# Performance work log

Measured on AMD Instinct MI355X. Metric: run time of the kernel, lower is better.

The kernel has to match this reference:

```python
import jax, jax.numpy as jnp
import numpy as np

B, K, D, H, V = 4096, 64, 128, 2048, 10000
EPS = 1e-5


def _project_ball(x):
    # map arbitrary vectors strictly inside the unit Poincare ball
    n = jnp.linalg.norm(x, axis=-1, keepdims=True)
    return 0.9 * x / (1.0 + n)


def setup_inputs() -> dict:
    key = jax.random.key(0)
    ks = jax.random.split(key, 12)
    type_embeddings = _project_ball(jax.random.normal(ks[0], (B, D), jnp.float32))
    neighbor_indexes = jax.random.randint(ks[1], (B, K), 0, V, jnp.int32)
    one_hot_neighbor_types = jnp.round(jax.random.uniform(ks[2], (B, K), jnp.float32))
    frequencies = jax.random.randint(ks[3], (V,), 1, 100000).astype(jnp.float32)
    type_lut = _project_ball(jax.random.normal(ks[4], (V, D), jnp.float32))
    IN = D + K * (D + 4 + 1)  # 8640
    s = 0.02
    W1 = jax.random.normal(ks[5], (IN, H), jnp.float32) * s
    b1 = jnp.zeros((H,), jnp.float32)
    Wh1 = jax.random.normal(ks[6], (H, H), jnp.float32) * s
    bh1 = jnp.zeros((H,), jnp.float32)
    Wh2 = jax.random.normal(ks[7], (H, H), jnp.float32) * s
    bh2 = jnp.zeros((H,), jnp.float32)
    W2 = jax.random.normal(ks[8], (H, K), jnp.float32) * s
    b2 = jnp.zeros((K,), jnp.float32)
    return dict(type_embeddings=type_embeddings, neighbor_indexes=neighbor_indexes,
                one_hot_neighbor_types=one_hot_neighbor_types, frequencies=frequencies,
                type_lut=type_lut, W1=W1, b1=b1, Wh1=Wh1, bh1=bh1, Wh2=Wh2, bh2=bh2,
                W2=W2, b2=b2)


def _forward(type_embeddings, neighbor_indexes, one_hot_neighbor_types, frequencies,
             type_lut, W1, b1, Wh1, bh1, Wh2, bh2, W2, b2):
    # embedding gather: [B, K, D]
    v = type_lut[neighbor_indexes]
    u = type_embeddings[:, None, :]  # [B, 1, D] broadcasts against [B, K, D]

    # extra features, all [B, K]
    squ = jnp.sum(u * u, axis=-1)
    sqv = jnp.sum(v * v, axis=-1)
    diff = u - v
    sqdist = jnp.sum(diff * diff, axis=-1)
    x = 1.0 + 2.0 * sqdist / ((1.0 - squ) * (1.0 - sqv))
    x = jnp.maximum(x, 1.0 + EPS)
    poincare = jnp.log(x + jnp.sqrt(x * x - 1.0))  # arccosh(x)

    dot = jnp.sum(u * v, axis=-1)
    cos = dot / jnp.maximum(jnp.sqrt(squ) * jnp.sqrt(sqv), 1e-8)
    summ = u + v
    polarization = (jnp.sum(summ * summ, axis=-1) - sqdist) / 4.0

    popularity = jnp.log1p(frequencies[neighbor_indexes])  # vectorized gather + log1p

    extra = jnp.stack([poincare, cos, polarization, dot], axis=-1)  # [B, K, 4]
    neighbor_rep = jnp.concatenate([v, extra, popularity[..., None]], axis=-1)  # [B, K, D+5]
    neighbor_rep = neighbor_rep.reshape(type_embeddings.shape[0], -1)
    inp = jnp.concatenate([type_embeddings, neighbor_rep], axis=-1)  # [B, D+K*(D+5)]

    h = jax.nn.relu(inp @ W1 + b1)        # dropout is identity at eval
    h = jax.nn.relu(h @ Wh1 + bh1)
    h = jax.nn.relu(h @ Wh2 + bh2)
    logits = h @ W2 + b2                  # [B, K]
    distribution = jax.nn.sigmoid(logits)

    t = one_hot_neighbor_types
    # stable BCE-with-logits, mean reduction
    loss = jnp.mean(jnp.maximum(logits, 0.0) - logits * t + jnp.log1p(jnp.exp(-jnp.abs(logits))))
    return distribution, loss


def reference(type_embeddings, neighbor_indexes, one_hot_neighbor_types, frequencies,
              type_lut, W1, b1, Wh1, bh1, Wh2, bh2, W2, b2):
    return _forward(type_embeddings, neighbor_indexes, one_hot_neighbor_types, frequencies,
                    type_lut, W1, b1, Wh1, bh1, Wh2, bh2, W2, b2)
```

## Files before the change

kernel.cpp:

```cpp
#include <hip/hip_runtime.h>

typedef unsigned short u16;
typedef unsigned int   u32;
typedef __attribute__((ext_vector_type(8))) __bf16 bf16x8;
typedef __attribute__((ext_vector_type(4))) float  f32x4;
typedef __attribute__((ext_vector_type(4))) u32    u32x4;

#define AS1 __attribute__((address_space(1)))
#define AS3 __attribute__((address_space(3)))


__device__ __forceinline__ u16 f2bf(float f) {
  return __builtin_bit_cast(u16, (__bf16)f);
}
__device__ __forceinline__ u32 pk2(float x, float y) {
  return (u32)__builtin_bit_cast(u16, (__bf16)x) |
         ((u32)__builtin_bit_cast(u16, (__bf16)y) << 16);
}

__device__ __forceinline__ float wred(float v) {
#pragma unroll
  for (int off = 32; off > 0; off >>= 1) v += __shfl_xor(v, off, 64);
  return v;
}

__device__ __forceinline__ void stage16(const u16* g, u16* l) {
  __builtin_amdgcn_global_load_lds((const AS1 void*)g, (AS3 void*)l, 16, 0, 0);
}

__device__ __forceinline__ int w1_orig_row(int p) {
  if (p < 128) return p;
  if (p < 8320) { int q = p - 128;  return 128 + (q >> 7) * 133 + (q & 127); }
  if (p < 8576) { int q = p - 8320; return 128 + (q >> 2) * 133 + 128 + (q & 3); }
  return 128 + (p - 8576) * 133 + 132;
}

__device__ __forceinline__ void w1_tile(const float* __restrict__ in,
                                        u16* __restrict__ out, int tile,
                                        u16 (*ls)[68], int t)
{
  const int p0 = (tile >> 5) << 6;
  const int h0 = (tile & 31) << 6;
  const int hl = t & 63, q = t >> 6;
  float v[16];
#pragma unroll
  for (int i = 0; i < 16; i++) {
    int pl = q * 16 + i;
    int orig = w1_orig_row(p0 + pl);
    v[i] = in[(size_t)orig * 2048 + h0 + hl];
  }
#pragma unroll
  for (int i = 0; i < 4; i++) {
    uint2 pk;
    pk.x = pk2(v[i * 4 + 0], v[i * 4 + 1]);
    pk.y = pk2(v[i * 4 + 2], v[i * 4 + 3]);
    *(uint2*)&ls[hl][q * 16 + i * 4] = pk;
  }
  __syncthreads();
  const int pp = t & 15, hq = t >> 4;
#pragma unroll
  for (int i = 0; i < 4; i++) {
    int hc = i * 16 + hq;
    uint2 vv = *(const uint2*)&ls[hc][pp * 4];
    *(uint2*)&out[(size_t)(h0 + hc) * 8640 + p0 + pp * 4] = vv;
  }
}

__device__ __forceinline__ void conv_tile(const float* __restrict__ in,
                                          u16* __restrict__ out, int R, int C,
                                          int tile, u16 (*ls)[68], int t)
{
  const int tiles_c = C >> 6;
  const int r0 = (tile / tiles_c) << 6;
  const int c0 = (tile % tiles_c) << 6;
  const int cl = t & 63, q = t >> 6;
  float v[16];
#pragma unroll
  for (int i = 0; i < 16; i++) {
    int rl = q * 16 + i;
    v[i] = in[(size_t)(r0 + rl) * C + c0 + cl];
  }
#pragma unroll
  for (int i = 0; i < 4; i++) {
    uint2 pk;
    pk.x = pk2(v[i * 4 + 0], v[i * 4 + 1]);
    pk.y = pk2(v[i * 4 + 2], v[i * 4 + 3]);
    *(uint2*)&ls[cl][q * 16 + i * 4] = pk;
  }
  __syncthreads();
  const int pp = t & 15, cq = t >> 4;
#pragma unroll
  for (int i = 0; i < 4; i++) {
    int cc = i * 16 + cq;
    uint2 vv = *(const uint2*)&ls[cc][pp * 4];
    *(uint2*)&out[(size_t)(c0 + cc) * R + r0 + pp * 4] = vv;
  }
}

__global__ __launch_bounds__(256) void prep_kernel(
    const float* __restrict__ W1,  u16* __restrict__ w1t,
    const float* __restrict__ Wh1, u16* __restrict__ wh1t,
    const float* __restrict__ Wh2, u16* __restrict__ wh2t,
    const float* __restrict__ W2,  u16* __restrict__ w2t,
    const float* __restrict__ te, const int* __restrict__ nidx,
    const float* __restrict__ freq, const float* __restrict__ lut,
    u16* __restrict__ inp)
{
  __shared__ u16 ls[64][68];
  __shared__ float u_sh[128];
  __shared__ float squ_sh;
  const int bid = blockIdx.x, t = threadIdx.x;
  if (bid < 4320)      { w1_tile(W1, w1t, bid, ls, t); return; }
  if (bid < 5344)      { conv_tile(Wh1, wh1t, 2048, 2048, bid - 4320, ls, t); return; }
  if (bid < 6368)      { conv_tile(Wh2, wh2t, 2048, 2048, bid - 5344, ls, t); return; }
  if (bid < 6400)      { conv_tile(W2,  w2t,  2048, 64,   bid - 6368, ls, t); return; }

  const int b = bid - 6400;
  const int l = t & 63, w = t >> 6;
  if (t < 128) u_sh[t] = te[(size_t)b * 128 + t];
  __syncthreads();
  if (w == 0) {
    float p = u_sh[l] * u_sh[l] + u_sh[l + 64] * u_sh[l + 64];
    p = wred(p);
    if (l == 0) squ_sh = p;
  }
  const size_t rb = (size_t)b * 8640;
  if (t < 64) {
    float2 u2 = *(const float2*)&u_sh[t * 2];
    *(u32*)&inp[rb + t * 2] = pk2(u2.x, u2.y);
  }
  __syncthreads();

  const float squ = squ_sh;
  const float rsq = 1.0f - squ;
  const float2 u2 = *(const float2*)&u_sh[l * 2];

#pragma unroll
  for (int mk = 0; mk < 4; ++mk) {
    const int kbase = w * 16 + mk * 4;
    int idx[4]; float2 v2[4]; float sqv[4], dot[4];
#pragma unroll
    for (int j = 0; j < 4; j++) {
      idx[j] = nidx[b * 64 + kbase + j];
      v2[j] = *(const float2*)&lut[(size_t)idx[j] * 128 + l * 2];
    }
#pragma unroll
    for (int j = 0; j < 4; j++) {
      sqv[j] = v2[j].x * v2[j].x + v2[j].y * v2[j].y;
      dot[j] = u2.x * v2[j].x + u2.y * v2[j].y;
    }
#pragma unroll
    for (int off = 32; off > 0; off >>= 1) {
#pragma unroll
      for (int j = 0; j < 4; j++) {
        sqv[j] += __shfl_xor(sqv[j], off, 64);
        dot[j] += __shfl_xor(dot[j], off, 64);
      }
    }
#pragma unroll
    for (int j = 0; j < 4; j++)
      *(u32*)&inp[rb + 128 + (size_t)(kbase + j) * 128 + l * 2] = pk2(v2[j].x, v2[j].y);

    const int js = l & 3;
    const float sv = (js & 2) ? ((js & 1) ? sqv[3] : sqv[2]) : ((js & 1) ? sqv[1] : sqv[0]);
    const float dt = (js & 2) ? ((js & 1) ? dot[3] : dot[2]) : ((js & 1) ? dot[1] : dot[0]);
    const int   ix = (js & 2) ? ((js & 1) ? idx[3] : idx[2]) : ((js & 1) ? idx[1] : idx[0]);
    const float sqd = squ + sv - 2.0f * dt;
    float x = 1.0f + 2.0f * sqd / (rsq * (1.0f - sv));
    x = fmaxf(x, 1.0f + 1e-5f);
    const float poin = logf(x + sqrtf(x * x - 1.0f));
    const float cosv = dt / fmaxf(sqrtf(squ * sv), 1e-8f);
    if (l < 4) {
      *(u32*)&inp[rb + 8320 + (kbase + l) * 4]     = pk2(poin, cosv);
      *(u32*)&inp[rb + 8320 + (kbase + l) * 4 + 2] = pk2(dt, dt);
      inp[rb + 8576 + kbase + l] = f2bf(log1pf(freq[ix]));
    }
  }
}

__global__ __launch_bounds__(256, 2) void gemm2b(
    const u16* __restrict__ A, const u16* __restrict__ BT,
    const float* __restrict__ bias, u16* __restrict__ out,
    int N, int Kd)
{
  extern __shared__ u16 lds[];
  const int t = threadIdx.x, l = t & 63, w = t >> 6;
  const int nb = N >> 7;
  const int cpx = gridDim.x >> 3;
  const int bid = (blockIdx.x & 7) * cpx + (blockIdx.x >> 3);
  const int bm = bid / nb, bn = bid % nb;
  const int m0 = bm << 7, n0 = bn << 7;
  const int vm = w >> 1, vn = w & 1;

  const size_t lda = (size_t)Kd;
  const int NT = Kd >> 6;

  const int sr = l >> 3;
  const int q  = (l & 7) ^ sr;
  const u16* sA = A  + (size_t)(m0 + w * 32 + sr) * lda + q * 8;
  const u16* sB = BT + (size_t)(n0 + w * 32 + sr) * lda + q * 8;
  const int dW = w * 2048;

  const int rl = l & 15;
  const int c0 = ((0 + (l >> 4)) ^ (rl & 7)) * 8;
  const int c1 = ((4 + (l >> 4)) ^ (rl & 7)) * 8;
  const int aBase = (vm * 64 + rl) * 64;
  const int bBase = 8192 + (vn * 64 + rl) * 64;

  f32x4 acc[4][4] = {};
  bf16x8 a0[4], a1[4], b0[4], b1[4];

  auto stageT = [&](int o, int tt) {
    const size_t kt = (size_t)tt * 64;
#pragma unroll
    for (int i = 0; i < 4; i++) {
      stage16(sA + (size_t)i * 8 * lda + kt, lds + o + dW + i * 512);
      stage16(sB + (size_t)i * 8 * lda + kt, lds + o + 8192 + dW + i * 512);
    }
  };
  auto mmq = [&](const bf16x8* a, const bf16x8* b) {
    __builtin_amdgcn_s_setprio(1);
#pragma unroll
    for (int mi = 0; mi < 4; mi++)
#pragma unroll
      for (int ni = 0; ni < 4; ni++)
        acc[mi][ni] = __builtin_amdgcn_mfma_f32_16x16x32_bf16(a[mi], b[ni], acc[mi][ni], 0, 0, 0);
    __builtin_amdgcn_s_setprio(0);
  };

  stageT(0, 0);

  for (int ti = 0; ti < NT; ++ti) {
    const int o  = (ti & 1) ? 16384 : 0;
    const int on = o ^ 16384;
    asm volatile("s_waitcnt vmcnt(0)" ::: "memory");
    __builtin_amdgcn_s_barrier();
#pragma unroll
    for (int x = 0; x < 4; x++) b0[x] = *(const bf16x8*)&lds[o + bBase + x * 1024 + c0];
#pragma unroll
    for (int x = 0; x < 4; x++) a0[x] = *(const bf16x8*)&lds[o + aBase + x * 1024 + c0];
#pragma unroll
    for (int x = 0; x < 4; x++) b1[x] = *(const bf16x8*)&lds[o + bBase + x * 1024 + c1];
#pragma unroll
    for (int x = 0; x < 4; x++) a1[x] = *(const bf16x8*)&lds[o + aBase + x * 1024 + c1];
    if (ti + 1 < NT) stageT(on, ti + 1);
    asm volatile("s_waitcnt lgkmcnt(8)" ::: "memory");
    __builtin_amdgcn_sched_barrier(0);
    mmq(a0, b0);
    asm volatile("s_waitcnt lgkmcnt(0)" ::: "memory");
    __builtin_amdgcn_sched_barrier(0);
    mmq(a1, b1);
  }

  const int rq = l >> 4, rl2 = l & 15;
#pragma unroll
  for (int mi = 0; mi < 4; mi++) {
#pragma unroll
    for (int ni = 0; ni < 4; ni++) {
      const int col = n0 + vn * 64 + ni * 16 + rl2;
      const float bv = bias[col];
#pragma unroll
      for (int j = 0; j < 4; j++) {
        const int row = m0 + vm * 64 + mi * 16 + rq * 4 + j;
        float vv = acc[mi][ni][j] + bv;
        out[(size_t)row * N + col] = f2bf(fmaxf(vv, 0.0f));
      }
    }
  }
}

__global__ __launch_bounds__(256, 2) void gemm4_part(
    const u16* __restrict__ A, const u16* __restrict__ BT,
    float* __restrict__ pbuf)
{
  __shared__ u16 lsA[2 * 128 * 32];
  __shared__ u16 lsB[2 * 64 * 32];
  const int t = threadIdx.x, l = t & 63, w = t >> 6;
  const int bmx = blockIdx.x & 31, sk = blockIdx.x >> 5;
  const int m0 = bmx << 7, k0 = sk << 9;
  float* pout = pbuf + (size_t)sk * 262144;
  const int wm = w >> 1, wn = w & 1;

  f32x4 acc[4][2] = {};
  const int srow = l >> 2, scol = (l & 3) * 8;

  const u16* pA0 = A  + (size_t)(m0 + w * 16 + srow)      * 2048 + scol + k0;
  const u16* pA1 = A  + (size_t)(m0 + 64 + w * 16 + srow) * 2048 + scol + k0;
  const u16* pB0 = BT + (size_t)(w * 16 + srow)           * 2048 + scol + k0;

  auto stage = [&](int buf, int kt) {
    u16* dA = lsA + buf * 4096;
    u16* dB = lsB + buf * 2048;
    stage16(pA0 + kt, dA + w * 512);
    stage16(pA1 + kt, dA + 2048 + w * 512);
    stage16(pB0 + kt, dB + w * 512);
  };

  stage(0, 0);
  __syncthreads();

  const int kk = (l >> 4) * 8;
  const int rl = l & 15;
  int cur = 0;
  for (int kt = 0; kt < 512; kt += 32) {
    if (kt + 32 < 512) stage(cur ^ 1, kt + 32);
    const u16* sA = lsA + cur * 4096;
    const u16* sB = lsB + cur * 2048;
    bf16x8 a[4], bb[2];
#pragma unroll
    for (int mi = 0; mi < 4; mi++)
      a[mi] = *(const bf16x8*)&sA[(wm * 64 + mi * 16 + rl) * 32 + kk];
#pragma unroll
    for (int ni = 0; ni < 2; ni++)
      bb[ni] = *(const bf16x8*)&sB[(wn * 32 + ni * 16 + rl) * 32 + kk];
#pragma unroll
    for (int mi = 0; mi < 4; mi++)
#pragma unroll
      for (int ni = 0; ni < 2; ni++)
        acc[mi][ni] = __builtin_amdgcn_mfma_f32_16x16x32_bf16(a[mi], bb[ni], acc[mi][ni], 0, 0, 0);
    __syncthreads();
    cur ^= 1;
  }

  const int rq = l >> 4, rl2 = l & 15;
#pragma unroll
  for (int mi = 0; mi < 4; mi++)
#pragma unroll
    for (int ni = 0; ni < 2; ni++) {
      const int col = wn * 32 + ni * 16 + rl2;
#pragma unroll
      for (int j = 0; j < 4; j++) {
        const int row = m0 + wm * 64 + mi * 16 + rq * 4 + j;
        pout[(size_t)row * 64 + col] = acc[mi][ni][j];
      }
    }
}

__global__ __launch_bounds__(256) void gemm4_combine(
    const float* __restrict__ pbuf, const float* __restrict__ bias,
    const float* __restrict__ oneh, float* __restrict__ dist,
    float* __restrict__ part2)
{
  __shared__ float red[256];
  const int t = threadIdx.x;
  const size_t base = (size_t)blockIdx.x * 1024 + t * 4;
  f32x4 s = *(const f32x4*)&pbuf[base];
  s += *(const f32x4*)&pbuf[base + 262144];
  s += *(const f32x4*)&pbuf[base + 524288];
  s += *(const f32x4*)&pbuf[base + 786432];
  const int col0 = (int)(base & 63);
  f32x4 th = *(const f32x4*)&oneh[base];
  float lsum = 0.0f;
  f32x4 dv;
#pragma unroll
  for (int j = 0; j < 4; j++) {
    const float x = s[j] + bias[col0 + j];
    dv[j] = 1.0f / (1.0f + expf(-x));
    lsum += fmaxf(x, 0.0f) - x * th[j] + log1pf(expf(-fabsf(x)));
  }
  *(f32x4*)&dist[base] = dv;
  red[t] = lsum;
  __syncthreads();
  for (int s2 = 128; s2 > 0; s2 >>= 1) {
    if (t < s2) red[t] += red[t + s2];
    __syncthreads();
  }
  if (t == 0) part2[blockIdx.x] = red[0];
}

__global__ void loss_final(const float* __restrict__ part2, float* __restrict__ outloss) {
  const int l = threadIdx.x;
  float v = 0.0f;
#pragma unroll
  for (int i = 0; i < 4; i++) v += part2[l + i * 64];
  v = wred(v);
  if (l == 0) outloss[0] = v * (1.0f / 262144.0f);
}

extern "C" void kernel_launch(void* const* d_in, const int* in_sizes, int n_in,
                              void* d_out, int out_size, void* d_ws, size_t ws_size,
                              hipStream_t stream)
{
  const float* te   = (const float*)d_in[0];
  const int*   nidx = (const int*)  d_in[1];
  const float* oneh = (const float*)d_in[2];
  const float* freq = (const float*)d_in[3];
  const float* lut  = (const float*)d_in[4];
  const float* W1   = (const float*)d_in[5];
  const float* b1   = (const float*)d_in[6];
  const float* Wh1  = (const float*)d_in[7];
  const float* bh1  = (const float*)d_in[8];
  const float* Wh2  = (const float*)d_in[9];
  const float* bh2  = (const float*)d_in[10];
  const float* W2   = (const float*)d_in[11];
  const float* b2   = (const float*)d_in[12];

  float* dist  = (float*)d_out;
  float* lossp = dist + 262144;

  size_t off = 0;
  char* base = (char*)d_ws;
  auto alloc = [&](size_t bytes) { char* p = base + off; off += (bytes + 255) & ~(size_t)255; return p; };
  u16* inp   = (u16*)alloc((size_t)4096 * 8640 * 2);
  u16* w1t   = (u16*)alloc((size_t)2048 * 8640 * 2);
  u16* wh1t  = (u16*)alloc((size_t)2048 * 2048 * 2);
  u16* wh2t  = (u16*)alloc((size_t)2048 * 2048 * 2);
  u16* w2t   = (u16*)alloc((size_t)64 * 2048 * 2);
  u16* h1    = (u16*)alloc((size_t)4096 * 2048 * 2);
  float* part2 = (float*)alloc(1024);
  u16* h2 = inp;
  u16* h3 = w1t;
  float* pbuf = (float*)wh1t;
  if (off > ws_size) return;

  (void)hipFuncSetAttribute((const void*)gemm2b,
                            hipFuncAttributeMaxDynamicSharedMemorySize, 65536);

  prep_kernel<<<10496, 256, 0, stream>>>(W1, w1t, Wh1, wh1t, Wh2, wh2t, W2, w2t,
                                         te, nidx, freq, lut, inp);

  gemm2b<<<512, 256, 65536, stream>>>(inp, w1t, b1, h1, 2048, 8640);
  gemm2b<<<512, 256, 65536, stream>>>(h1, wh1t, bh1, h2, 2048, 2048);
  gemm2b<<<512, 256, 65536, stream>>>(h2, wh2t, bh2, h3, 2048, 2048);
  gemm4_part   <<<128, 256, 0, stream>>>(h3, w2t, pbuf);
  gemm4_combine<<<256, 256, 0, stream>>>(pbuf, b2, oneh, dist, part2);
  loss_final   <<<1, 64, 0, stream>>>(part2, lossp);
}
```

Measured before the change: 268.1 us.

## Split K across wave pairs in GEMM tile with LDS reduction

```diff
diff --git a/kernel.cpp b/kernel.cpp
--- a/kernel.cpp
+++ b/kernel.cpp
@@ -178,7 +178,7 @@
   }
 }
 
-__global__ __launch_bounds__(256, 2) void gemm2b(
+__global__ __launch_bounds__(256, 2) void gemm2k(
     const u16* __restrict__ A, const u16* __restrict__ BT,
     const float* __restrict__ bias, u16* __restrict__ out,
     int N, int Kd)
@@ -190,7 +190,7 @@
   const int bid = (blockIdx.x & 7) * cpx + (blockIdx.x >> 3);
   const int bm = bid / nb, bn = bid % nb;
   const int m0 = bm << 7, n0 = bn << 7;
-  const int vm = w >> 1, vn = w & 1;
+  const int kg = w >> 1, vn = w & 1;
 
   const size_t lda = (size_t)Kd;
   const int NT = Kd >> 6;
@@ -202,13 +202,12 @@
   const int dW = w * 2048;
 
   const int rl = l & 15;
-  const int c0 = ((0 + (l >> 4)) ^ (rl & 7)) * 8;
-  const int c1 = ((4 + (l >> 4)) ^ (rl & 7)) * 8;
-  const int aBase = (vm * 64 + rl) * 64;
+  const int cK = ((kg * 4 + (l >> 4)) ^ (rl & 7)) * 8;
+  const int aBase = rl * 64;
   const int bBase = 8192 + (vn * 64 + rl) * 64;
 
-  f32x4 acc[4][4] = {};
-  bf16x8 a0[4], a1[4], b0[4], b1[4];
+  f32x4 acc[8][4] = {};
+  bf16x8 a[8], b[4];
 
   auto stageT = [&](int o, int tt) {
     const size_t kt = (size_t)tt * 64;
@@ -217,15 +216,6 @@
       stage16(sA + (size_t)i * 8 * lda + kt, lds + o + dW + i * 512);
       stage16(sB + (size_t)i * 8 * lda + kt, lds + o + 8192 + dW + i * 512);
     }
-  };
-  auto mmq = [&](const bf16x8* a, const bf16x8* b) {
-    __builtin_amdgcn_s_setprio(1);
-#pragma unroll
-    for (int mi = 0; mi < 4; mi++)
-#pragma unroll
-      for (int ni = 0; ni < 4; ni++)
-        acc[mi][ni] = __builtin_amdgcn_mfma_f32_16x16x32_bf16(a[mi], b[ni], acc[mi][ni], 0, 0, 0);
-    __builtin_amdgcn_s_setprio(0);
   };
 
   stageT(0, 0);
@@ -236,34 +226,55 @@
     asm volatile("s_waitcnt vmcnt(0)" ::: "memory");
     __builtin_amdgcn_s_barrier();
 #pragma unroll
-    for (int x = 0; x < 4; x++) b0[x] = *(const bf16x8*)&lds[o + bBase + x * 1024 + c0];
-#pragma unroll
-    for (int x = 0; x < 4; x++) a0[x] = *(const bf16x8*)&lds[o + aBase + x * 1024 + c0];
-#pragma unroll
-    for (int x = 0; x < 4; x++) b1[x] = *(const bf16x8*)&lds[o + bBase + x * 1024 + c1];
-#pragma unroll
-    for (int x = 0; x < 4; x++) a1[x] = *(const bf16x8*)&lds[o + aBase + x * 1024 + c1];
+    for (int x = 0; x < 4; x++) b[x] = *(const bf16x8*)&lds[o + bBase + x * 1024 + cK];
+#pragma unroll
+    for (int x = 0; x < 8; x++) a[x] = *(const bf16x8*)&lds[o + aBase + x * 1024 + cK];
     if (ti + 1 < NT) stageT(on, ti + 1);
     asm volatile("s_waitcnt lgkmcnt(8)" ::: "memory");
     __builtin_amdgcn_sched_barrier(0);
-    mmq(a0, b0);
+    __builtin_amdgcn_s_setprio(1);
+#pragma unroll
+    for (int mi = 0; mi < 4; mi++)
+#pragma unroll
+      for (int ni = 0; ni < 4; ni++)
+        acc[mi][ni] = __builtin_amdgcn_mfma_f32_16x16x32_bf16(a[mi], b[ni], acc[mi][ni], 0, 0, 0);
+    __builtin_amdgcn_s_setprio(0);
     asm volatile("s_waitcnt lgkmcnt(0)" ::: "memory");
     __builtin_amdgcn_sched_barrier(0);
-    mmq(a1, b1);
-  }
-
-  const int rq = l >> 4, rl2 = l & 15;
-#pragma unroll
-  for (int mi = 0; mi < 4; mi++) {
-#pragma unroll
-    for (int ni = 0; ni < 4; ni++) {
-      const int col = n0 + vn * 64 + ni * 16 + rl2;
-      const float bv = bias[col];
-#pragma unroll
-      for (int j = 0; j < 4; j++) {
-        const int row = m0 + vm * 64 + mi * 16 + rq * 4 + j;
-        float vv = acc[mi][ni][j] + bv;
-        out[(size_t)row * N + col] = f2bf(fmaxf(vv, 0.0f));
+    __builtin_amdgcn_s_setprio(1);
+#pragma unroll
+    for (int mi = 4; mi < 8; mi++)
+#pragma unroll
+      for (int ni = 0; ni < 4; ni++)
+        acc[mi][ni] = __builtin_amdgcn_mfma_f32_16x16x32_bf16(a[mi], b[ni], acc[mi][ni], 0, 0, 0);
+    __builtin_amdgcn_s_setprio(0);
+  }
+
+  __syncthreads();
+  float* pl = (float*)lds;
+  if (kg == 1) {
+#pragma unroll
+    for (int mi = 0; mi < 8; mi++)
+#pragma unroll
+      for (int ni = 0; ni < 4; ni++)
+        *(f32x4*)&pl[vn * 8192 + (mi * 4 + ni) * 256 + l * 4] = acc[mi][ni];
+  }
+  __syncthreads();
+  if (kg == 0) {
+    const int rq = l >> 4, rl2 = l & 15;
+#pragma unroll
+    for (int mi = 0; mi < 8; mi++) {
+#pragma unroll
+      for (int ni = 0; ni < 4; ni++) {
+        f32x4 p2 = *(const f32x4*)&pl[vn * 8192 + (mi * 4 + ni) * 256 + l * 4];
+        const int col = n0 + vn * 64 + ni * 16 + rl2;
+        const float bv = bias[col];
+#pragma unroll
+        for (int j = 0; j < 4; j++) {
+          const int row = m0 + mi * 16 + rq * 4 + j;
+          float vv = acc[mi][ni][j] + p2[j] + bv;
+          out[(size_t)row * N + col] = f2bf(fmaxf(vv, 0.0f));
+        }
       }
     }
   }
@@ -413,15 +424,15 @@
   float* pbuf = (float*)wh1t;
   if (off > ws_size) return;
 
-  (void)hipFuncSetAttribute((const void*)gemm2b,
+  (void)hipFuncSetAttribute((const void*)gemm2k,
                             hipFuncAttributeMaxDynamicSharedMemorySize, 65536);
 
   prep_kernel<<<10496, 256, 0, stream>>>(W1, w1t, Wh1, wh1t, Wh2, wh2t, W2, w2t,
                                          te, nidx, freq, lut, inp);
 
-  gemm2b<<<512, 256, 65536, stream>>>(inp, w1t, b1, h1, 2048, 8640);
-  gemm2b<<<512, 256, 65536, stream>>>(h1, wh1t, bh1, h2, 2048, 2048);
-  gemm2b<<<512, 256, 65536, stream>>>(h2, wh2t, bh2, h3, 2048, 2048);
+  gemm2k<<<512, 256, 65536, stream>>>(inp, w1t, b1, h1, 2048, 8640);
+  gemm2k<<<512, 256, 65536, stream>>>(h1, wh1t, bh1, h2, 2048, 2048);
+  gemm2k<<<512, 256, 65536, stream>>>(h2, wh2t, bh2, h3, 2048, 2048);
   gemm4_part   <<<128, 256, 0, stream>>>(h3, w2t, pbuf);
   gemm4_combine<<<256, 256, 0, stream>>>(pbuf, b2, oneh, dist, part2);
   loss_final   <<<1, 64, 0, stream>>>(part2, lossp);
```

After: 266.7 us (median of 2 runs). About the same (-0.5%).
